# Performance work log

Hardware: AMD Instinct MI355X
Metric: run time of the kernel (lower is better)

Reference implementation:

```python
import jax, jax.numpy as jnp
import numpy as np

N_NODES = 50000
N_EDGES = 1600000
N_GRAPHS = 64
NEG_SLOPE = 0.2  # PyG GATConv default leaky_relu slope


def gat_conv(x, src, dst, W, a_src, a_dst, bias, heads, ch, concat):
    N = x.shape[0]
    h = (x @ W).reshape(N, heads, ch)                      # [N,H,C]
    alpha_s = (h * a_src).sum(-1)                          # [N,H]
    alpha_d = (h * a_dst).sum(-1)                          # [N,H]
    e = jax.nn.leaky_relu(alpha_s[src] + alpha_d[dst], NEG_SLOPE)  # [E,H]
    # segment softmax grouped by destination node
    emax = jax.ops.segment_max(e, dst, num_segments=N)
    e = jnp.exp(e - emax[dst])
    denom = jax.ops.segment_sum(e, dst, num_segments=N)
    alpha = e / (denom[dst] + 1e-16)                       # [E,H]
    out = jax.ops.segment_sum(h[src] * alpha[:, :, None], dst, num_segments=N)  # [N,H,C]
    out = out.reshape(N, heads * ch) if concat else out.mean(axis=1)
    return out + bias


def setup_inputs() -> dict:
    key = jax.random.key(0)
    ks = jax.random.split(key, 12)
    x = jax.random.normal(ks[0], (N_NODES, 512), dtype=jnp.float32)
    edge_index = jax.random.randint(ks[1], (2, N_EDGES), 0, N_NODES, dtype=jnp.int64 if jax.config.jax_enable_x64 else jnp.int32)
    batch = jnp.sort(jax.random.randint(ks[2], (N_NODES,), 0, N_GRAPHS))
    s1 = 1.0 / np.sqrt(512)
    s2 = 1.0 / np.sqrt(64)
    return {
        "x": x,
        "edge_index": edge_index,
        "batch": batch,
        "W1": jax.random.uniform(ks[3], (512, 64), jnp.float32, -s1, s1),
        "att_src1": jax.random.uniform(ks[4], (8, 8), jnp.float32, -1, 1) * 0.3,
        "att_dst1": jax.random.uniform(ks[5], (8, 8), jnp.float32, -1, 1) * 0.3,
        "bias1": jnp.zeros((64,), jnp.float32),
        "W2": jax.random.uniform(ks[6], (64, 32), jnp.float32, -s2, s2),
        "att_src2": jax.random.uniform(ks[7], (1, 32), jnp.float32, -1, 1) * 0.3,
        "att_dst2": jax.random.uniform(ks[8], (1, 32), jnp.float32, -1, 1) * 0.3,
        "bias2": jnp.zeros((32,), jnp.float32),
        "lin_w": jax.random.uniform(ks[9], (32, 2), jnp.float32, -1.0 / np.sqrt(32), 1.0 / np.sqrt(32)),
        "lin_b": jnp.zeros((2,), jnp.float32),
    }


def reference(x, edge_index, batch, W1, att_src1, att_dst1, bias1, W2, att_src2, att_dst2, bias2, lin_w, lin_b):
    N = x.shape[0]
    loop = jnp.arange(N, dtype=edge_index.dtype)
    src = jnp.concatenate([edge_index[0], loop])  # PyG add_self_loops=True
    dst = jnp.concatenate([edge_index[1], loop])
    # dropout layers are identity in eval mode
    h = gat_conv(x, src, dst, W1, att_src1, att_dst1, bias1, heads=8, ch=8, concat=True)
    h = jax.nn.elu(h)
    h = gat_conv(h, src, dst, W2, att_src2, att_dst2, bias2, heads=1, ch=32, concat=False)
    # global mean pool over graphs
    sums = jax.ops.segment_sum(h, batch, num_segments=N_GRAPHS)
    counts = jax.ops.segment_sum(jnp.ones((N, 1), h.dtype), batch, num_segments=N_GRAPHS)
    pooled = sums / jnp.maximum(counts, 1.0)
    return pooled @ lin_w + lin_b
```

## Files before the change

kernel.cpp:

```cpp
#include <hip/hip_runtime.h>
#include <cstdint>
#include <cstddef>

#define NN 50000
#define NE 1600000
#define ET (NE + NN)
#define NG 64
#define SCAN_BLOCKS ((NN + 255) / 256)
#define NB ((NN + 127) >> 7)
#define CAP 6144
#define EPT 16
#define EPB (256 * EPT)
#define BIN_BLOCKS ((ET + EPB - 1) / EPB)
#define GEMM1_BLOCKS ((NN + 63) / 64)
#define WFRAG_BLOCKS 16

typedef __attribute__((ext_vector_type(8))) short short8v;
typedef __attribute__((ext_vector_type(4))) float f32x4;

__device__ inline unsigned short f2bf(float f) {
    unsigned u = __float_as_uint(f);
    u += 0x7fffu + ((u >> 16) & 1u);
    return (unsigned short)(u >> 16);
}

__global__ __launch_bounds__(256) void k_f0(
    const int* __restrict__ esrc, const int* __restrict__ edst,
    int* __restrict__ gcnt, unsigned* __restrict__ rec,
    const float* __restrict__ W1, unsigned short* __restrict__ w1f,
    const int* __restrict__ batch, int* __restrict__ lo) {
    __shared__ int bcnt[NB];
    int bid = blockIdx.x, tid = threadIdx.x;
    if (bid < BIN_BLOCKS) {
        for (int b = tid; b < NB; b += 256) bcnt[b] = 0;
        __syncthreads();
        int e0 = bid * EPB;
        unsigned rv[EPT]; int bk[EPT]; int rk[EPT];
#pragma unroll
        for (int q = 0; q < EPT; ++q) {
            int e = e0 + q * 256 + tid;
            rk[q] = -1;
            if (e < ET) {
                int s, d;
                if (e < NE) { s = esrc[e]; d = edst[e]; } else { s = d = e - NE; }
                rv[q] = ((unsigned)s << 7) | (unsigned)(d & 127);
                bk[q] = d >> 7;
                rk[q] = atomicAdd(&bcnt[bk[q]], 1);
            }
        }
        __syncthreads();
        for (int b = tid; b < NB; b += 256)
            bcnt[b] = atomicAdd(&gcnt[b], bcnt[b]);
        __syncthreads();
#pragma unroll
        for (int q = 0; q < EPT; ++q) {
            if (rk[q] >= 0) rec[(size_t)bk[q] * CAP + bcnt[bk[q]] + rk[q]] = rv[q];
        }
    } else if (bid < BIN_BLOCKS + WFRAG_BLOCKS) {
        int slot = (bid - BIN_BLOCKS) * 256 + tid;
        int S = slot >> 8;
        int ct = (slot >> 6) & 3;
        int l = slot & 63;
        int kb = S * 32 + ((l >> 4) << 3);
        int c = ct * 16 + (l & 15);
        unsigned short* dst = w1f + (size_t)slot * 8;
#pragma unroll
        for (int j = 0; j < 8; ++j)
            dst[j] = f2bf(W1[(kb + j) * 64 + c]);
    } else {
        int n = (bid - BIN_BLOCKS - WFRAG_BLOCKS) * 256 + tid;
        if (n >= NN) return;
        int b = batch[n];
        if (n == 0) {
            for (int g = 0; g <= b; ++g) lo[g] = 0;
        } else {
            int pb = batch[n - 1];
            for (int g = pb + 1; g <= b; ++g) lo[g] = n;
        }
        if (n == NN - 1) {
            for (int g = b + 1; g <= NG; ++g) lo[g] = NN;
        }
    }
}

__global__ __launch_bounds__(256, 8) void k_f1(
    const int* __restrict__ gcnt, const unsigned* __restrict__ rec,
    int* __restrict__ obeg, int* __restrict__ oend, int* __restrict__ csr,
    const float* __restrict__ x, const unsigned short* __restrict__ w1f,
    const float* __restrict__ aS, const float* __restrict__ aD,
    unsigned short* __restrict__ h1b, float* __restrict__ as1, float* __restrict__ ad1) {
    __shared__ int sm[256];
    int bid = blockIdx.x, t = threadIdx.x;

    if (bid < NB) {
        int* cnt  = sm;
        int* lcur = sm + 128;
        int b = bid, tid = t;
        if (tid < 128) cnt[tid] = 0;
        __syncthreads();
        size_t base = (size_t)b * CAP;
        int nrec = gcnt[b];
        for (int i = tid; i < nrec; i += 256)
            atomicAdd(&cnt[rec[base + i] & 127], 1);
        __syncthreads();
        int v = 0, incl = 0;
        if (tid < 128) {
            int lane = tid & 63;
            v = cnt[tid];
            incl = v;
#pragma unroll
            for (int ofs = 1; ofs < 64; ofs <<= 1) {
                int o = __shfl_up(incl, ofs);
                if (lane >= ofs) incl += o;
            }
            cnt[tid] = incl;
        }
        __syncthreads();
        if (tid < 128) {
            int ex = incl - v + ((tid >= 64) ? cnt[63] : 0);
            int n = (b << 7) + tid;
            int pos = (int)base + ex;
            if (n < NN) { obeg[n] = pos; oend[n] = pos + v; }
            lcur[tid] = pos;
        }
        __syncthreads();
        for (int i = tid; i < nrec; i += 256) {
            unsigned r = rec[base + i];
            int pos = atomicAdd(&lcur[r & 127], 1);
            csr[pos] = (int)(r >> 7);
        }
    } else {
        int w = t >> 6, l = t & 63;
        int n0 = (bid - NB) * 64;
        int rrow = n0 + w * 16 + (l & 15);
        int rc = (rrow < NN) ? rrow : (NN - 1);
        const float* __restrict__ xr = x + (size_t)rc * 512;
        const short8v* __restrict__ wv8 = reinterpret_cast<const short8v*>(w1f);

        f32x4 acc0 = {0.f, 0.f, 0.f, 0.f};
        f32x4 acc1 = {0.f, 0.f, 0.f, 0.f};
        f32x4 acc2 = {0.f, 0.f, 0.f, 0.f};
        f32x4 acc3 = {0.f, 0.f, 0.f, 0.f};

        int lk = (l >> 4) << 3;
#pragma unroll 4
        for (int s = 0; s < 16; ++s) {
            int k0 = s * 32 + lk;
            const float4* xp = reinterpret_cast<const float4*>(xr + k0);
            float4 a0 = xp[0];
            float4 a1 = xp[1];
            short8v af;
            af[0] = (short)f2bf(a0.x); af[1] = (short)f2bf(a0.y);
            af[2] = (short)f2bf(a0.z); af[3] = (short)f2bf(a0.w);
            af[4] = (short)f2bf(a1.x); af[5] = (short)f2bf(a1.y);
            af[6] = (short)f2bf(a1.z); af[7] = (short)f2bf(a1.w);
            const short8v* bp = wv8 + (size_t)(s * 4) * 64 + l;
            short8v bf0 = bp[0];
            short8v bf1 = bp[64];
            short8v bf2 = bp[128];
            short8v bf3 = bp[192];
            acc0 = __builtin_amdgcn_mfma_f32_16x16x32_bf16(af, bf0, acc0, 0, 0, 0);
            acc1 = __builtin_amdgcn_mfma_f32_16x16x32_bf16(af, bf1, acc1, 0, 0, 0);
            acc2 = __builtin_amdgcn_mfma_f32_16x16x32_bf16(af, bf2, acc2, 0, 0, 0);
            acc3 = __builtin_amdgcn_mfma_f32_16x16x32_bf16(af, bf3, acc3, 0, 0, 0);
        }

        int hi = (l & 15) >> 3;
        int cc = l & 7;
#pragma unroll
        for (int reg = 0; reg < 4; ++reg) {
            int row16 = ((l >> 4) << 2) + reg;
            int r = n0 + w * 16 + row16;
            float v0 = acc0[reg], v1 = acc1[reg], v2 = acc2[reg], v3 = acc3[reg];
            if (r < NN) {
                unsigned short* hp = h1b + (size_t)r * 64 + (l & 15);
                hp[0]  = f2bf(v0);
                hp[16] = f2bf(v1);
                hp[32] = f2bf(v2);
                hp[48] = f2bf(v3);
            }
            float ps[4], pd[4];
            float vv[4] = {v0, v1, v2, v3};
#pragma unroll
            for (int ct = 0; ct < 4; ++ct) {
                int h = ct * 2 + hi;
                ps[ct] = vv[ct] * aS[h * 8 + cc];
                pd[ct] = vv[ct] * aD[h * 8 + cc];
            }
#pragma unroll
            for (int ofs = 1; ofs <= 4; ofs <<= 1) {
#pragma unroll
                for (int ct = 0; ct < 4; ++ct) {
                    ps[ct] += __shfl_xor(ps[ct], ofs);
                    pd[ct] += __shfl_xor(pd[ct], ofs);
                }
            }
            if (cc == 0 && r < NN) {
#pragma unroll
                for (int ct = 0; ct < 4; ++ct) {
                    int h = ct * 2 + hi;
                    as1[r * 8 + h] = ps[ct];
                    ad1[r * 8 + h] = pd[ct];
                }
            }
        }
    }
}

__global__ __launch_bounds__(256) void k_agg1g(
    const int* __restrict__ obeg, const int* __restrict__ oend, const int* __restrict__ csr,
    const unsigned short* __restrict__ h1b, const float* __restrict__ as1, const float* __restrict__ ad1,
    const float* __restrict__ bias1, const float* __restrict__ W2,
    const float* __restrict__ aS2, const float* __restrict__ aD2,
    unsigned short* __restrict__ h2b, float* __restrict__ as2, float* __restrict__ ad2) {
    __shared__ float w2l[64 * 32];
    __shared__ float h1ol[4][64];
    int tid = threadIdx.x;
    for (int i = tid; i < 2048; i += 256) w2l[i] = W2[i];
    __syncthreads();

    int l = tid & 63;
    int wv = tid >> 6;
    int dst = blockIdx.x * 4 + wv;
    if (dst >= NN) return;
    int g = l >> 4;
    int q = l & 15;
    int h = q >> 1;
    int beg = obeg[dst], end = oend[dst];
    int lastj = end - 1;
    float adh = ad1[dst * 8 + h];
    const uint2* __restrict__ h1u = reinterpret_cast<const uint2*>(h1b);

    float4 acc = make_float4(0.f, 0.f, 0.f, 0.f);
    float dsum = 0.f;

    int sA[4], sB[4];
#pragma unroll
    for (int p = 0; p < 4; ++p) sA[p] = csr[min(beg + p * 4 + g, lastj)];
    for (int j = beg; j < end; j += 16) {
#pragma unroll
        for (int p = 0; p < 4; ++p) sB[p] = csr[min(j + 16 + p * 4 + g, lastj)];
        float av[4]; uint2 vv[4];
#pragma unroll
        for (int p = 0; p < 4; ++p) {
            av[p] = as1[sA[p] * 8 + h];
            vv[p] = h1u[(size_t)sA[p] * 16 + q];
        }
#pragma unroll
        for (int p = 0; p < 4; ++p) {
            float e = av[p] + adh; e = (e > 0.f) ? e : 0.2f * e;
            float w = __expf(e);
            w = (j + p * 4 + g < end) ? w : 0.f;
            float x0 = __uint_as_float(vv[p].x << 16);
            float x1 = __uint_as_float(vv[p].x & 0xffff0000u);
            float x2 = __uint_as_float(vv[p].y << 16);
            float x3 = __uint_as_float(vv[p].y & 0xffff0000u);
            acc.x += w * x0; acc.y += w * x1;
            acc.z += w * x2; acc.w += w * x3;
            dsum += w;
        }
#pragma unroll
        for (int p = 0; p < 4; ++p) sA[p] = sB[p];
    }

#pragma unroll
    for (int ofs = 16; ofs <= 32; ofs <<= 1) {
        acc.x += __shfl_xor(acc.x, ofs);
        acc.y += __shfl_xor(acc.y, ofs);
        acc.z += __shfl_xor(acc.z, ofs);
        acc.w += __shfl_xor(acc.w, ofs);
        dsum  += __shfl_xor(dsum, ofs);
    }

    if (g == 0) {
        float inv = 1.f / (dsum + 1e-16f);
        const float4 bq = reinterpret_cast<const float4*>(bias1)[q];
        float4 r;
        r.x = acc.x * inv + bq.x;
        r.y = acc.y * inv + bq.y;
        r.z = acc.z * inv + bq.z;
        r.w = acc.w * inv + bq.w;
        r.x = (r.x > 0.f) ? r.x : (__expf(r.x) - 1.f);
        r.y = (r.y > 0.f) ? r.y : (__expf(r.y) - 1.f);
        r.z = (r.z > 0.f) ? r.z : (__expf(r.z) - 1.f);
        r.w = (r.w > 0.f) ? r.w : (__expf(r.w) - 1.f);
        h1ol[wv][q * 4 + 0] = r.x;
        h1ol[wv][q * 4 + 1] = r.y;
        h1ol[wv][q * 4 + 2] = r.z;
        h1ol[wv][q * 4 + 3] = r.w;
    }

    int c = l & 31, half = l >> 5;
    const float* hrow = h1ol[wv];
    float acc2 = 0.f;
#pragma unroll 8
    for (int kk = 0; kk < 32; ++kk) {
        int k = half * 32 + kk;
        acc2 += hrow[k] * w2l[k * 32 + c];
    }
    acc2 += __shfl_xor(acc2, 32);
    if (l < 32) h2b[(size_t)dst * 32 + c] = f2bf(acc2);
    float ps = acc2 * aS2[c], pd = acc2 * aD2[c];
#pragma unroll
    for (int ofs = 1; ofs <= 16; ofs <<= 1) {
        ps += __shfl_xor(ps, ofs);
        pd += __shfl_xor(pd, ofs);
    }
    if (l == 0) { as2[dst] = ps; ad2[dst] = pd; }
}

__global__ __launch_bounds__(256) void k_agg2(
    const int* __restrict__ obeg, const int* __restrict__ oend, const int* __restrict__ csr,
    const unsigned short* __restrict__ h2b, const float* __restrict__ as2, const float* __restrict__ ad2,
    const float* __restrict__ bias2, float* __restrict__ o2) {
    int l = threadIdx.x & 63;
    int dst = blockIdx.x * 4 + (threadIdx.x >> 6);
    if (dst >= NN) return;
    int g = l >> 3;
    int q = l & 7;
    int beg = obeg[dst], end = oend[dst];
    int lastj = end - 1;
    float adh = ad2[dst];
    const uint2* __restrict__ h2u = reinterpret_cast<const uint2*>(h2b);

    float4 acc = make_float4(0.f, 0.f, 0.f, 0.f);
    float dsum = 0.f;

    int sA[4], sB[4];
#pragma unroll
    for (int p = 0; p < 4; ++p) sA[p] = csr[min(beg + p * 8 + g, lastj)];
    for (int j = beg; j < end; j += 32) {
#pragma unroll
        for (int p = 0; p < 4; ++p) sB[p] = csr[min(j + 32 + p * 8 + g, lastj)];
        float av[4]; uint2 vv[4];
#pragma unroll
        for (int p = 0; p < 4; ++p) {
            av[p] = as2[sA[p]];
            vv[p] = h2u[(size_t)sA[p] * 8 + q];
        }
#pragma unroll
        for (int p = 0; p < 4; ++p) {
            float e = av[p] + adh; e = (e > 0.f) ? e : 0.2f * e;
            float w = __expf(e);
            w = (j + p * 8 + g < end) ? w : 0.f;
            float x0 = __uint_as_float(vv[p].x << 16);
            float x1 = __uint_as_float(vv[p].x & 0xffff0000u);
            float x2 = __uint_as_float(vv[p].y << 16);
            float x3 = __uint_as_float(vv[p].y & 0xffff0000u);
            acc.x += w * x0; acc.y += w * x1;
            acc.z += w * x2; acc.w += w * x3;
            dsum += w;
        }
#pragma unroll
        for (int p = 0; p < 4; ++p) sA[p] = sB[p];
    }

#pragma unroll
    for (int ofs = 8; ofs <= 32; ofs <<= 1) {
        acc.x += __shfl_xor(acc.x, ofs);
        acc.y += __shfl_xor(acc.y, ofs);
        acc.z += __shfl_xor(acc.z, ofs);
        acc.w += __shfl_xor(acc.w, ofs);
        dsum  += __shfl_xor(dsum, ofs);
    }

    if (g == 0) {
        float inv = 1.f / (dsum + 1e-16f);
        const float4 bq = reinterpret_cast<const float4*>(bias2)[q];
        float4 r;
        r.x = acc.x * inv + bq.x;
        r.y = acc.y * inv + bq.y;
        r.z = acc.z * inv + bq.z;
        r.w = acc.w * inv + bq.w;
        reinterpret_cast<float4*>(o2)[dst * 8 + q] = r;
    }
}

__global__ __launch_bounds__(256) void k_pool(const float* __restrict__ o2, const int* __restrict__ lo,
                                              float* __restrict__ pooled) {
    __shared__ float red[256];
    int g = blockIdx.x & 63, q = blockIdx.x >> 6;
    int beg = lo[g], end = lo[g + 1];
    int c = threadIdx.x & 31, row = threadIdx.x >> 5;
    float s = 0.f;
    for (int n = beg + q * 8 + row; n < end; n += 32) s += o2[n * 32 + c];
    red[threadIdx.x] = s;
    __syncthreads();
    for (int rr = 4; rr >= 1; rr >>= 1) {
        if (row < rr) red[threadIdx.x] += red[(row + rr) * 32 + c];
        __syncthreads();
    }
    if (row == 0) atomicAdd(&pooled[g * 32 + c], red[c]);
}

__global__ void k_fin(const float* __restrict__ pooled, const int* __restrict__ lo,
                      const float* __restrict__ lw, const float* __restrict__ lb,
                      float* __restrict__ out) {
    int t = threadIdx.x;
    if (t >= 128) return;
    int g = t >> 1, o = t & 1;
    int cnt = lo[g + 1] - lo[g];
    float inv = 1.f / fmaxf((float)cnt, 1.f);
    float s = 0.f;
#pragma unroll
    for (int c = 0; c < 32; ++c) s += pooled[g * 32 + c] * lw[c * 2 + o];
    out[g * 2 + o] = s * inv + lb[o];
}

extern "C" void kernel_launch(void* const* d_in, const int* in_sizes, int n_in,
                              void* d_out, int out_size, void* d_ws, size_t ws_size,
                              hipStream_t stream) {
    const float* x   = (const float*)d_in[0];
    const int*   ei  = (const int*)d_in[1];
    const int*   bat = (const int*)d_in[2];
    const float* W1  = (const float*)d_in[3];
    const float* aS1 = (const float*)d_in[4];
    const float* aD1 = (const float*)d_in[5];
    const float* b1  = (const float*)d_in[6];
    const float* W2  = (const float*)d_in[7];
    const float* aS2 = (const float*)d_in[8];
    const float* aD2 = (const float*)d_in[9];
    const float* b2  = (const float*)d_in[10];
    const float* lw  = (const float*)d_in[11];
    const float* lb  = (const float*)d_in[12];
    float* out = (float*)d_out;

    const int* esrc = ei;
    const int* edst = ei + NE;

    char* ws = (char*)d_ws;
    size_t off = 0;
    auto alloc = [&](size_t bytes) -> void* {
        off = (off + 255) & ~(size_t)255;
        void* p = ws + off;
        off += bytes;
        return p;
    };

    unsigned short* h1b = (unsigned short*)alloc((size_t)NN * 64 * 2);
    unsigned short* h2b = (unsigned short*)alloc((size_t)NN * 32 * 2);
    float* o2   = (float*)alloc((size_t)NN * 32 * 4);
    float* as1  = (float*)alloc((size_t)NN * 8 * 4);
    float* ad1  = (float*)alloc((size_t)NN * 8 * 4);
    float* as2  = (float*)alloc((size_t)NN * 4);
    float* ad2  = (float*)alloc((size_t)NN * 4);
    int*   obeg = (int*)alloc((size_t)NN * 4);
    int*   oend = (int*)alloc((size_t)NN * 4);
    int*   csr  = (int*)alloc((size_t)NB * CAP * 4);
    unsigned* rec = (unsigned*)alloc((size_t)NB * CAP * 4);
    int*   gcnt = (int*)alloc((size_t)NB * 4);
    unsigned short* w1f = (unsigned short*)alloc((size_t)512 * 64 * 2);
    float* pooled = (float*)alloc((size_t)NG * 32 * 4);
    int*   lo   = (int*)alloc((size_t)(NG + 1) * 4);
    if (off > ws_size) return;

    hipMemsetAsync(gcnt, 0, (size_t)NB * 4, stream);
    hipMemsetAsync(pooled, 0, (size_t)NG * 32 * 4, stream);

    k_f0<<<BIN_BLOCKS + WFRAG_BLOCKS + SCAN_BLOCKS, 256, 0, stream>>>(
        esrc, edst, gcnt, rec, W1, w1f, bat, lo);
    k_f1<<<NB + GEMM1_BLOCKS, 256, 0, stream>>>(
        gcnt, rec, obeg, oend, csr, x, w1f, aS1, aD1, h1b, as1, ad1);

    k_agg1g<<<(NN + 3) / 4, 256, 0, stream>>>(obeg, oend, csr, h1b, as1, ad1, b1,
                                              W2, aS2, aD2, h2b, as2, ad2);
    k_agg2<<<(NN + 3) / 4, 256, 0, stream>>>(obeg, oend, csr, h2b, as2, ad2, b2, o2);

    k_pool<<<NG * 4, 256, 0, stream>>>(o2, lo, pooled);
    k_fin<<<1, 128, 0, stream>>>(pooled, lo, lw, lb, out);
}
```

Measured before the change: 151.5 us.

## Split layer-1 GEMM across binning and CSR-build kernels to overlap work

Moves the W1 bf16 fragment conversion into its own small kernel, then splits the 782 GEMM1 blocks in half: one half runs alongside the edge-binning pass and the other alongside the CSR scatter pass. The aim is to balance the two fused kernels so the compute-bound GEMM overlaps the memory- and atomic-bound graph construction instead of sitting entirely in the second kernel. It adds one more kernel launch, and removes the occupancy hint from the second kernel.

```diff
diff --git a/kernel.cpp b/kernel.cpp
--- a/kernel.cpp
+++ b/kernel.cpp
@@ -12,8 +12,7 @@
 #define EPT 16
 #define EPB (256 * EPT)
 #define BIN_BLOCKS ((ET + EPB - 1) / EPB)
-#define GEMM1_BLOCKS ((NN + 63) / 64)
-#define WFRAG_BLOCKS 16
+#define G1H 391
 
 typedef __attribute__((ext_vector_type(8))) short short8v;
 typedef __attribute__((ext_vector_type(4))) float f32x4;
@@ -24,17 +23,114 @@
     return (unsigned short)(u >> 16);
 }
 
-__global__ __launch_bounds__(256) void k_f0(
+__device__ __forceinline__ void gemm1_block(
+    int n0, int t,
+    const float* __restrict__ x, const unsigned short* __restrict__ w1f,
+    const float* __restrict__ aS, const float* __restrict__ aD,
+    unsigned short* __restrict__ h1b, float* __restrict__ as1, float* __restrict__ ad1) {
+    int w = t >> 6, l = t & 63;
+    int rrow = n0 + w * 16 + (l & 15);
+    int rc = (rrow < NN) ? rrow : (NN - 1);
+    const float* __restrict__ xr = x + (size_t)rc * 512;
+    const short8v* __restrict__ wv8 = reinterpret_cast<const short8v*>(w1f);
+
+    f32x4 acc0 = {0.f, 0.f, 0.f, 0.f};
+    f32x4 acc1 = {0.f, 0.f, 0.f, 0.f};
+    f32x4 acc2 = {0.f, 0.f, 0.f, 0.f};
+    f32x4 acc3 = {0.f, 0.f, 0.f, 0.f};
+
+    int lk = (l >> 4) << 3;
+#pragma unroll 4
+    for (int s = 0; s < 16; ++s) {
+        const float4* xp = reinterpret_cast<const float4*>(xr + s * 32 + lk);
+        float4 a0 = xp[0];
+        float4 a1 = xp[1];
+        short8v af;
+        af[0] = (short)f2bf(a0.x); af[1] = (short)f2bf(a0.y);
+        af[2] = (short)f2bf(a0.z); af[3] = (short)f2bf(a0.w);
+        af[4] = (short)f2bf(a1.x); af[5] = (short)f2bf(a1.y);
+        af[6] = (short)f2bf(a1.z); af[7] = (short)f2bf(a1.w);
+        const short8v* bp = wv8 + (size_t)(s * 4) * 64 + l;
+        short8v bf0 = bp[0];
+        short8v bf1 = bp[64];
+        short8v bf2 = bp[128];
+        short8v bf3 = bp[192];
+        acc0 = __builtin_amdgcn_mfma_f32_16x16x32_bf16(af, bf0, acc0, 0, 0, 0);
+        acc1 = __builtin_amdgcn_mfma_f32_16x16x32_bf16(af, bf1, acc1, 0, 0, 0);
+        acc2 = __builtin_amdgcn_mfma_f32_16x16x32_bf16(af, bf2, acc2, 0, 0, 0);
+        acc3 = __builtin_amdgcn_mfma_f32_16x16x32_bf16(af, bf3, acc3, 0, 0, 0);
+    }
+
+    int hi = (l & 15) >> 3;
+    int cc = l & 7;
+#pragma unroll
+    for (int reg = 0; reg < 4; ++reg) {
+        int row16 = ((l >> 4) << 2) + reg;
+        int r = n0 + w * 16 + row16;
+        float v0 = acc0[reg], v1 = acc1[reg], v2 = acc2[reg], v3 = acc3[reg];
+        if (r < NN) {
+            unsigned short* hp = h1b + (size_t)r * 64 + (l & 15);
+            hp[0]  = f2bf(v0);
+            hp[16] = f2bf(v1);
+            hp[32] = f2bf(v2);
+            hp[48] = f2bf(v3);
+        }
+        float ps[4], pd[4];
+        float vv[4] = {v0, v1, v2, v3};
+#pragma unroll
+        for (int ct = 0; ct < 4; ++ct) {
+            int h = ct * 2 + hi;
+            ps[ct] = vv[ct] * aS[h * 8 + cc];
+            pd[ct] = vv[ct] * aD[h * 8 + cc];
+        }
+#pragma unroll
+        for (int ofs = 1; ofs <= 4; ofs <<= 1) {
+#pragma unroll
+            for (int ct = 0; ct < 4; ++ct) {
+                ps[ct] += __shfl_xor(ps[ct], ofs);
+                pd[ct] += __shfl_xor(pd[ct], ofs);
+            }
+        }
+        if (cc == 0 && r < NN) {
+#pragma unroll
+            for (int ct = 0; ct < 4; ++ct) {
+                int h = ct * 2 + hi;
+                as1[r * 8 + h] = ps[ct];
+                ad1[r * 8 + h] = pd[ct];
+            }
+        }
+    }
+}
+
+__global__ __launch_bounds__(256) void k_wf(const float* __restrict__ W1,
+                                            unsigned short* __restrict__ w1f) {
+    int slot = blockIdx.x * 256 + threadIdx.x;
+    int S = slot >> 8;
+    int ct = (slot >> 6) & 3;
+    int l = slot & 63;
+    int kb = S * 32 + ((l >> 4) << 3);
+    int c = ct * 16 + (l & 15);
+    unsigned short* dst = w1f + (size_t)slot * 8;
+#pragma unroll
+    for (int j = 0; j < 8; ++j)
+        dst[j] = f2bf(W1[(kb + j) * 64 + c]);
+}
+
+__global__ __launch_bounds__(256) void k_fa(
+    const float* __restrict__ x, const unsigned short* __restrict__ w1f,
+    const float* __restrict__ aS, const float* __restrict__ aD,
+    unsigned short* __restrict__ h1b, float* __restrict__ as1, float* __restrict__ ad1,
     const int* __restrict__ esrc, const int* __restrict__ edst,
     int* __restrict__ gcnt, unsigned* __restrict__ rec,
-    const float* __restrict__ W1, unsigned short* __restrict__ w1f,
     const int* __restrict__ batch, int* __restrict__ lo) {
     __shared__ int bcnt[NB];
     int bid = blockIdx.x, tid = threadIdx.x;
-    if (bid < BIN_BLOCKS) {
+    if (bid < G1H) {
+        gemm1_block(bid * 64, tid, x, w1f, aS, aD, h1b, as1, ad1);
+    } else if (bid < G1H + BIN_BLOCKS) {
         for (int b = tid; b < NB; b += 256) bcnt[b] = 0;
         __syncthreads();
-        int e0 = bid * EPB;
+        int e0 = (bid - G1H) * EPB;
         unsigned rv[EPT]; int bk[EPT]; int rk[EPT];
 #pragma unroll
         for (int q = 0; q < EPT; ++q) {
@@ -56,19 +152,8 @@
         for (int q = 0; q < EPT; ++q) {
             if (rk[q] >= 0) rec[(size_t)bk[q] * CAP + bcnt[bk[q]] + rk[q]] = rv[q];
         }
-    } else if (bid < BIN_BLOCKS + WFRAG_BLOCKS) {
-        int slot = (bid - BIN_BLOCKS) * 256 + tid;
-        int S = slot >> 8;
-        int ct = (slot >> 6) & 3;
-        int l = slot & 63;
-        int kb = S * 32 + ((l >> 4) << 3);
-        int c = ct * 16 + (l & 15);
-        unsigned short* dst = w1f + (size_t)slot * 8;
-#pragma unroll
-        for (int j = 0; j < 8; ++j)
-            dst[j] = f2bf(W1[(kb + j) * 64 + c]);
     } else {
-        int n = (bid - BIN_BLOCKS - WFRAG_BLOCKS) * 256 + tid;
+        int n = (bid - G1H - BIN_BLOCKS) * 256 + tid;
         if (n >= NN) return;
         int b = batch[n];
         if (n == 0) {
@@ -83,19 +168,20 @@
     }
 }
 
-__global__ __launch_bounds__(256, 8) void k_f1(
-    const int* __restrict__ gcnt, const unsigned* __restrict__ rec,
-    int* __restrict__ obeg, int* __restrict__ oend, int* __restrict__ csr,
+__global__ __launch_bounds__(256) void k_fb(
     const float* __restrict__ x, const unsigned short* __restrict__ w1f,
     const float* __restrict__ aS, const float* __restrict__ aD,
-    unsigned short* __restrict__ h1b, float* __restrict__ as1, float* __restrict__ ad1) {
+    unsigned short* __restrict__ h1b, float* __restrict__ as1, float* __restrict__ ad1,
+    const int* __restrict__ gcnt, const unsigned* __restrict__ rec,
+    int* __restrict__ obeg, int* __restrict__ oend, int* __restrict__ csr) {
     __shared__ int sm[256];
-    int bid = blockIdx.x, t = threadIdx.x;
-
-    if (bid < NB) {
+    int bid = blockIdx.x, tid = threadIdx.x;
+    if (bid < G1H) {
+        gemm1_block((G1H + bid) * 64, tid, x, w1f, aS, aD, h1b, as1, ad1);
+    } else {
         int* cnt  = sm;
         int* lcur = sm + 128;
-        int b = bid, tid = t;
+        int b = bid - G1H;
         if (tid < 128) cnt[tid] = 0;
         __syncthreads();
         size_t base = (size_t)b * CAP;
@@ -128,81 +214,6 @@
             unsigned r = rec[base + i];
             int pos = atomicAdd(&lcur[r & 127], 1);
             csr[pos] = (int)(r >> 7);
-        }
-    } else {
-        int w = t >> 6, l = t & 63;
-        int n0 = (bid - NB) * 64;
-        int rrow = n0 + w * 16 + (l & 15);
-        int rc = (rrow < NN) ? rrow : (NN - 1);
-        const float* __restrict__ xr = x + (size_t)rc * 512;
-        const short8v* __restrict__ wv8 = reinterpret_cast<const short8v*>(w1f);
-
-        f32x4 acc0 = {0.f, 0.f, 0.f, 0.f};
-        f32x4 acc1 = {0.f, 0.f, 0.f, 0.f};
-        f32x4 acc2 = {0.f, 0.f, 0.f, 0.f};
-        f32x4 acc3 = {0.f, 0.f, 0.f, 0.f};
-
-        int lk = (l >> 4) << 3;
-#pragma unroll 4
-        for (int s = 0; s < 16; ++s) {
-            int k0 = s * 32 + lk;
-            const float4* xp = reinterpret_cast<const float4*>(xr + k0);
-            float4 a0 = xp[0];
-            float4 a1 = xp[1];
-            short8v af;
-            af[0] = (short)f2bf(a0.x); af[1] = (short)f2bf(a0.y);
-            af[2] = (short)f2bf(a0.z); af[3] = (short)f2bf(a0.w);
-            af[4] = (short)f2bf(a1.x); af[5] = (short)f2bf(a1.y);
-            af[6] = (short)f2bf(a1.z); af[7] = (short)f2bf(a1.w);
-            const short8v* bp = wv8 + (size_t)(s * 4) * 64 + l;
-            short8v bf0 = bp[0];
-            short8v bf1 = bp[64];
-            short8v bf2 = bp[128];
-            short8v bf3 = bp[192];
-            acc0 = __builtin_amdgcn_mfma_f32_16x16x32_bf16(af, bf0, acc0, 0, 0, 0);
-            acc1 = __builtin_amdgcn_mfma_f32_16x16x32_bf16(af, bf1, acc1, 0, 0, 0);
-            acc2 = __builtin_amdgcn_mfma_f32_16x16x32_bf16(af, bf2, acc2, 0, 0, 0);
-            acc3 = __builtin_amdgcn_mfma_f32_16x16x32_bf16(af, bf3, acc3, 0, 0, 0);
-        }
-
-        int hi = (l & 15) >> 3;
-        int cc = l & 7;
-#pragma unroll
-        for (int reg = 0; reg < 4; ++reg) {
-            int row16 = ((l >> 4) << 2) + reg;
-            int r = n0 + w * 16 + row16;
-            float v0 = acc0[reg], v1 = acc1[reg], v2 = acc2[reg], v3 = acc3[reg];
-            if (r < NN) {
-                unsigned short* hp = h1b + (size_t)r * 64 + (l & 15);
-                hp[0]  = f2bf(v0);
-                hp[16] = f2bf(v1);
-                hp[32] = f2bf(v2);
-                hp[48] = f2bf(v3);
-            }
-            float ps[4], pd[4];
-            float vv[4] = {v0, v1, v2, v3};
-#pragma unroll
-            for (int ct = 0; ct < 4; ++ct) {
-                int h = ct * 2 + hi;
-                ps[ct] = vv[ct] * aS[h * 8 + cc];
-                pd[ct] = vv[ct] * aD[h * 8 + cc];
-            }
-#pragma unroll
-            for (int ofs = 1; ofs <= 4; ofs <<= 1) {
-#pragma unroll
-                for (int ct = 0; ct < 4; ++ct) {
-                    ps[ct] += __shfl_xor(ps[ct], ofs);
-                    pd[ct] += __shfl_xor(pd[ct], ofs);
-                }
-            }
-            if (cc == 0 && r < NN) {
-#pragma unroll
-                for (int ct = 0; ct < 4; ++ct) {
-                    int h = ct * 2 + hi;
-                    as1[r * 8 + h] = ps[ct];
-                    ad1[r * 8 + h] = pd[ct];
-                }
-            }
         }
     }
 }
@@ -457,10 +468,11 @@
     hipMemsetAsync(gcnt, 0, (size_t)NB * 4, stream);
     hipMemsetAsync(pooled, 0, (size_t)NG * 32 * 4, stream);
 
-    k_f0<<<BIN_BLOCKS + WFRAG_BLOCKS + SCAN_BLOCKS, 256, 0, stream>>>(
-        esrc, edst, gcnt, rec, W1, w1f, bat, lo);
-    k_f1<<<NB + GEMM1_BLOCKS, 256, 0, stream>>>(
-        gcnt, rec, obeg, oend, csr, x, w1f, aS1, aD1, h1b, as1, ad1);
+    k_wf<<<16, 256, 0, stream>>>(W1, w1f);
+    k_fa<<<G1H + BIN_BLOCKS + SCAN_BLOCKS, 256, 0, stream>>>(
+        x, w1f, aS1, aD1, h1b, as1, ad1, esrc, edst, gcnt, rec, bat, lo);
+    k_fb<<<G1H + NB, 256, 0, stream>>>(
+        x, w1f, aS1, aD1, h1b, as1, ad1, gcnt, rec, obeg, oend, csr);
 
     k_agg1g<<<(NN + 3) / 4, 256, 0, stream>>>(obeg, oend, csr, h1b, as1, ad1, b1,
                                               W2, aS2, aD2, h2b, as2, ad2);
```

Measured after the change: 148.8 us. No clear change (-1.8%).
